# Kernel optimization log

Hardware: AMD Instinct MI355X
Metric: run time of the kernel (lower is better)

## Reference

```python
import jax, jax.numpy as jnp
import numpy as np

N, E, F_IN, EDGE_DIM = 50000, 800000, 128, 64
H, C = 4, 64  # heads, per-head out channels
NEG_SLOPE = 0.2  # PyG GATConv default


def setup_inputs() -> dict:
    key = jax.random.key(0)
    ks = jax.random.split(key, 16)
    p = lambda i, shape: jax.random.normal(ks[i], shape, jnp.float32) * 0.05
    return {
        "node_features": jax.random.normal(ks[0], (N, F_IN), jnp.float32),
        "edge_features": jax.random.normal(ks[1], (E, EDGE_DIM), jnp.float32),
        "edge_index": jax.random.randint(ks[2], (2, E), 0, N),
        # layer 1 (concat=True, ELU)
        "W1": p(3, (F_IN, H * C)),
        "att_src1": p(4, (H, C)), "att_dst1": p(5, (H, C)), "att_edge1": p(6, (H, C)),
        "bias1": jnp.zeros((H * C,), jnp.float32),
        "edgeW1": p(7, (EDGE_DIM, H * C)),
        # layer 2 (concat=False -> mean over heads, no activation)
        "W2": p(8, (H * C, H * C)),
        "att_src2": p(9, (H, C)), "att_dst2": p(10, (H, C)), "att_edge2": p(11, (H, C)),
        "bias2": jnp.zeros((C,), jnp.float32),
        "edgeW2": p(12, (EDGE_DIM, H * C)),
    }


def _gat_layer(x, edge_feat, src, dst, W, a_s, a_d, a_e, bias, edgeW, concat):
    n = x.shape[0]
    h = (x @ W).reshape(n, H, C)                      # [N,H,C]
    ef = (edge_feat @ edgeW).reshape(-1, H, C)        # [E,H,C] edge_linear projection
    # GATConv add_self_loops=True, fill_value='mean': self-loop attr = mean of incoming edge attrs
    ones = jnp.ones((src.shape[0],), x.dtype)
    cnt = jnp.maximum(jax.ops.segment_sum(ones, dst, num_segments=n), 1.0)
    loop_attr = jax.ops.segment_sum(ef, dst, num_segments=n) / cnt[:, None, None]
    ef_f = jnp.concatenate([ef, loop_attr], axis=0)   # [E+N,H,C]
    loops = jnp.arange(n)
    src_f = jnp.concatenate([src, loops], axis=0)
    dst_f = jnp.concatenate([dst, loops], axis=0)
    # per-edge attention logits: alpha_j + alpha_i + alpha_edge
    a_src = jnp.einsum('nhc,hc->nh', h, a_s)
    a_dst = jnp.einsum('nhc,hc->nh', h, a_d)
    logits = a_src[src_f] + a_dst[dst_f] + jnp.einsum('ehc,hc->eh', ef_f, a_e)
    logits = jax.nn.leaky_relu(logits, NEG_SLOPE)     # [E+N,H]
    # segment softmax over incoming edges of each dst node (every node has a self-loop)
    m = jax.ops.segment_max(logits, dst_f, num_segments=n)
    pexp = jnp.exp(logits - m[dst_f])
    denom = jax.ops.segment_sum(pexp, dst_f, num_segments=n)
    alpha = pexp / (denom[dst_f] + 1e-16)
    # message = x_j * alpha, scatter-add to dst
    out = jax.ops.segment_sum(h[src_f] * alpha[..., None], dst_f, num_segments=n)  # [N,H,C]
    if concat:
        return out.reshape(n, H * C) + bias
    return out.mean(axis=1) + bias


def reference(node_features, edge_features, edge_index,
              W1, att_src1, att_dst1, att_edge1, bias1, edgeW1,
              W2, att_src2, att_dst2, att_edge2, bias2, edgeW2):
    src, dst = edge_index[0], edge_index[1]
    x = _gat_layer(node_features, edge_features, src, dst,
                   W1, att_src1, att_dst1, att_edge1, bias1, edgeW1, concat=True)
    x = jax.nn.elu(x)
    return _gat_layer(x, edge_features, src, dst,
                      W2, att_src2, att_dst2, att_edge2, bias2, edgeW2, concat=False)
```

## Files before the change

kernel.cpp:

```cpp
#include <hip/hip_runtime.h>
#include <hip/hip_fp16.h>
#include <math.h>

#define NNODE 50000
#define NEDGE 800000
#define FIN 128
#define EDIM 64
#define HC 256
#define NH 4
#define CC 64
#define SCAN_TILE 512

typedef _Float16 half8v __attribute__((ext_vector_type(8)));
typedef _Float16 half4v __attribute__((ext_vector_type(4)));
typedef float floatx4 __attribute__((ext_vector_type(4)));

__global__ __launch_bounds__(256) void k_prep(int* counts,
                                              const float* __restrict__ W1, _Float16* wt1,
                                              const float* __restrict__ W2, _Float16* wt2,
                                              const float* __restrict__ eW1, const float* __restrict__ ae1, float* we1,
                                              const float* __restrict__ eW2, const float* __restrict__ ae2, float* we2) {
    int b = blockIdx.x, t = threadIdx.x;
    if (b < 196) {
        int i = b * 256 + t;
        if (i < NNODE) counts[i] = 0;
    } else if (b < 324) {
        int idx = (b - 196) * 256 + t;
        int n = idx >> 7, k = idx & 127;
        wt1[n * FIN + k] = (_Float16)W1[(size_t)k * HC + n];
    } else if (b < 580) {
        int idx = (b - 324) * 256 + t;
        int n = idx >> 8, k = idx & 255;
        wt2[n * HC + k] = (_Float16)W2[(size_t)k * HC + n];
    } else {
        int idx = (b - 580) * 256 + t;
        const float* eW = idx < 256 ? eW1 : eW2;
        const float* ae = idx < 256 ? ae1 : ae2;
        float* we = idx < 256 ? we1 : we2;
        int q = idx & 255;
        int d = q >> 2, hh = q & 3;
        float s = 0.f;
        for (int c = 0; c < 64; c++) s += eW[d * HC + hh * 64 + c] * ae[hh * 64 + c];
        we[d * 4 + hh] = s;
    }
}

__global__ void k_count(const int* __restrict__ dst, int* counts, int* __restrict__ rank, int E) {
    int e = blockIdx.x * 256 + threadIdx.x;
    if (e < E) rank[e] = atomicAdd(&counts[dst[e]], 1);
}

__global__ void k_scan1(const int* __restrict__ counts, int* offs, int* tilesums, int N) {
    __shared__ int s[SCAN_TILE];
    int t = threadIdx.x;
    int i = blockIdx.x * SCAN_TILE + t;
    int v = (i < N) ? counts[i] : 0;
    s[t] = v;
    for (int off = 1; off < SCAN_TILE; off <<= 1) {
        __syncthreads();
        int x = (t >= off) ? s[t - off] : 0;
        __syncthreads();
        s[t] += x;
    }
    __syncthreads();
    if (i < N) offs[i] = s[t] - v;
    if (t == SCAN_TILE - 1) tilesums[blockIdx.x] = s[t];
}

__global__ void k_scan3(int* offs, const int* __restrict__ tilesums, int nt, int N, int E) {
    __shared__ int sT[128];
    int t = threadIdx.x;
    if (t < 128) sT[t] = (t < nt) ? tilesums[t] : 0;
    __syncthreads();
    int b = blockIdx.x;
    int pre = 0;
    for (int i = 0; i < b; i++) pre += sT[i];
    int i = b * SCAN_TILE + t;
    if (i < N) offs[i] += pre;
    if (b == 0 && t == 0) offs[N] = E;
}

__device__ inline float4 h4_to_f4(uint2 r) {
    float2 fa = __half22float2(*(__half2*)&r.x);
    float2 fb = __half22float2(*(__half2*)&r.y);
    return make_float4(fa.x, fa.y, fb.x, fb.y);
}

__device__ inline float sel_h(float4 v, int head) {
    return head == 0 ? v.x : head == 1 ? v.y : head == 2 ? v.z : v.w;
}

__global__ __launch_bounds__(256) void k_edge(const int* __restrict__ src,
                                              const int* __restrict__ dst,
                                              const int* __restrict__ rank,
                                              const int* __restrict__ offs,
                                              const float* __restrict__ ef,
                                              const float* __restrict__ we1,
                                              const float* __restrict__ we2,
                                              int* __restrict__ srcs,
                                              float* __restrict__ elogc1,
                                              float* __restrict__ elogc2, int E) {
    __shared__ float sw1[256], sw2[256];
    int t = threadIdx.x;
    sw1[t] = we1[t];
    sw2[t] = we2[t];
    __syncthreads();
    int lane = t & 63, wave = t >> 6;
    int g = lane >> 2, r = lane & 3;
    int e = blockIdx.x * 64 + wave * 16 + g;
    if (e >= E) return;

    const float4* row = (const float4*)(ef + (size_t)e * EDIM);
    float4 v0 = row[r * 4 + 0];
    float4 v1 = row[r * 4 + 1];
    float4 v2 = row[r * 4 + 2];
    float4 v3 = row[r * 4 + 3];

    int pos = offs[dst[e]] + rank[e];
    int sv = src[e];

    float a10 = 0.f, a11 = 0.f, a12 = 0.f, a13 = 0.f;
    float a20 = 0.f, a21 = 0.f, a22 = 0.f, a23 = 0.f;
    int c0 = r * 16;
    const float4* vv[4] = {&v0, &v1, &v2, &v3};
#pragma unroll
    for (int q = 0; q < 4; q++) {
        const float* vp = (const float*)vv[q];
#pragma unroll
        for (int k = 0; k < 4; k++) {
            float f = vp[k];
            int c = c0 + q * 4 + k;
            float4 w1 = *(const float4*)&sw1[c << 2];
            float4 w2 = *(const float4*)&sw2[c << 2];
            a10 += f * w1.x; a11 += f * w1.y; a12 += f * w1.z; a13 += f * w1.w;
            a20 += f * w2.x; a21 += f * w2.y; a22 += f * w2.z; a23 += f * w2.w;
        }
    }
#pragma unroll
    for (int msk = 1; msk <= 2; msk <<= 1) {
        a10 += __shfl_xor(a10, msk, 64); a11 += __shfl_xor(a11, msk, 64);
        a12 += __shfl_xor(a12, msk, 64); a13 += __shfl_xor(a13, msk, 64);
        a20 += __shfl_xor(a20, msk, 64); a21 += __shfl_xor(a21, msk, 64);
        a22 += __shfl_xor(a22, msk, 64); a23 += __shfl_xor(a23, msk, 64);
    }
    if (r == 0) ((float4*)elogc1)[pos] = make_float4(a10, a11, a12, a13);
    else if (r == 1) ((float4*)elogc2)[pos] = make_float4(a20, a21, a22, a23);
    else if (r == 2) srcs[pos] = sv;
}

template <typename AT>
__global__ __launch_bounds__(256) void k_gemm_mfma(const AT* __restrict__ A,
                                                   const _Float16* __restrict__ Wt16,
                                                   _Float16* __restrict__ H16,
                                                   const float* __restrict__ att_s,
                                                   const float* __restrict__ att_d,
                                                   float* __restrict__ asrc,
                                                   float* __restrict__ adst,
                                                   int M, int K) {
    int wave = threadIdx.x >> 6, lane = threadIdx.x & 63;
    int quad = lane >> 4, l16 = lane & 15;
    int row = blockIdx.x * 64 + wave * 16 + l16;
    bool rok = row < M;
    floatx4 acc[16];
#pragma unroll
    for (int i = 0; i < 16; i++) acc[i] = (floatx4)(0.0f);
    int nk = K >> 5;
    for (int kk = 0; kk < nk; kk++) {
        half8v a = {};
        if (rok) {
            if constexpr (sizeof(AT) == 2) {
                a = *(const half8v*)(A + (size_t)row * K + kk * 32 + quad * 8);
            } else {
                const float* ap = (const float*)A + (size_t)row * K + kk * 32 + quad * 8;
                float4 v0 = *(const float4*)ap;
                float4 v1 = *(const float4*)(ap + 4);
                a[0] = (_Float16)v0.x; a[1] = (_Float16)v0.y;
                a[2] = (_Float16)v0.z; a[3] = (_Float16)v0.w;
                a[4] = (_Float16)v1.x; a[5] = (_Float16)v1.y;
                a[6] = (_Float16)v1.z; a[7] = (_Float16)v1.w;
            }
        }
#pragma unroll
        for (int nt = 0; nt < 16; nt++) {
            half8v b = *(const half8v*)(Wt16 + (size_t)(nt * 16 + l16) * K + kk * 32 + quad * 8);
            acc[nt] = __builtin_amdgcn_mfma_f32_16x16x32_f16(a, b, acc[nt], 0, 0, 0);
        }
    }
    float asl[16], adl[16];
#pragma unroll
    for (int nt = 0; nt < 16; nt++) {
        asl[nt] = att_s[nt * 16 + l16];
        adl[nt] = att_d[nt * 16 + l16];
    }
    int orow0 = blockIdx.x * 64 + wave * 16 + quad * 4;
#pragma unroll
    for (int r = 0; r < 4; r++) {
        int orow = orow0 + r;
        float4 vs4, vd4;
        float* vsp = (float*)&vs4;
        float* vdp = (float*)&vd4;
#pragma unroll
        for (int hh = 0; hh < 4; hh++) {
            float vs = 0.f, vd = 0.f;
#pragma unroll
            for (int q = 0; q < 4; q++) {
                int nt = hh * 4 + q;
                float hv = acc[nt][r];
                vs += hv * asl[nt];
                vd += hv * adl[nt];
            }
            vs += __shfl_xor(vs, 1, 64); vd += __shfl_xor(vd, 1, 64);
            vs += __shfl_xor(vs, 2, 64); vd += __shfl_xor(vd, 2, 64);
            vs += __shfl_xor(vs, 4, 64); vd += __shfl_xor(vd, 4, 64);
            vs += __shfl_xor(vs, 8, 64); vd += __shfl_xor(vd, 8, 64);
            vsp[hh] = vs; vdp[hh] = vd;
        }
        if (l16 == 0 && orow < M) {
            ((float4*)asrc)[orow] = vs4;
            ((float4*)adst)[orow] = vd4;
        }
    }
#pragma unroll
    for (int r = 0; r < 4; r++) {
        int orow = orow0 + r;
        if (orow < M) {
#pragma unroll
            for (int nt = 0; nt < 16; nt++)
                H16[(size_t)orow * HC + nt * 16 + l16] = (_Float16)acc[nt][r];
        }
    }
}

template <int LAYER>
__global__ __launch_bounds__(256) void k_aggr_fused(const _Float16* __restrict__ hb,
                                                    const float* __restrict__ elogc,
                                                    const float* __restrict__ asrc,
                                                    const float* __restrict__ adst,
                                                    const int* __restrict__ offs,
                                                    const int* __restrict__ srcs,
                                                    const float* __restrict__ bias,
                                                    _Float16* __restrict__ out16,
                                                    float* __restrict__ out32, int N) {
    __shared__ float sW[4][256];
    int wave = threadIdx.x >> 6, lane = threadIdx.x & 63;
    int n = blockIdx.x * 4 + wave;
    if (n >= N) return;
    int head = lane >> 4;
    const uint2* hf = (const uint2*)hb;
    const float4* elc = (const float4*)elogc;
    const float4* asp = (const float4*)asrc;
    float* sWp = sW[wave];
    int beg = offs[n], end = offs[n + 1];

    float4 adn = ((const float4*)adst)[n];
    float adnh = sel_h(adn, head);

    float denom = 0.f;
    float sx = 0.f, sy = 0.f, sz = 0.f, sw = 0.f;
    float ax = 0.f, ay = 0.f, az = 0.f, aw = 0.f;

    for (int i0 = beg; i0 < end; i0 += 64) {
        int m = end - i0; if (m > 64) m = 64;
        bool act = lane < m;
        int sj = 0;
        float4 el = make_float4(0.f, 0.f, 0.f, 0.f);
        float4 a4 = make_float4(0.f, 0.f, 0.f, 0.f);
        if (act) {
            uint idx = (uint)(i0 + lane);
            sj = srcs[idx];
            el = elc[idx];
            a4 = asp[(uint)sj];
        }
        sx += el.x; sy += el.y; sz += el.z; sw += el.w;
        float4 w4;
        float l;
        l = a4.x + adn.x + el.x; l = l > 0.f ? l : 0.2f * l; w4.x = act ? __expf(l) : 0.f;
        l = a4.y + adn.y + el.y; l = l > 0.f ? l : 0.2f * l; w4.y = act ? __expf(l) : 0.f;
        l = a4.z + adn.z + el.z; l = l > 0.f ? l : 0.2f * l; w4.z = act ? __expf(l) : 0.f;
        l = a4.w + adn.w + el.w; l = l > 0.f ? l : 0.2f * l; w4.w = act ? __expf(l) : 0.f;
        *(float4*)&sWp[lane << 2] = w4;
        __builtin_amdgcn_wave_barrier();

        int j = 0;
        for (; j + 16 <= m; j += 16) {
            uint2 r[16];
            float w[16];
#pragma unroll
            for (int k = 0; k < 16; k++) {
                int sk = __builtin_amdgcn_readlane(sj, j + k);
                w[k] = sWp[((j + k) << 2) + head];
                r[k] = hf[(size_t)((uint)sk * 64u) + lane];
            }
#pragma unroll
            for (int k = 0; k < 16; k++) {
                float4 h4 = h4_to_f4(r[k]);
                denom += w[k];
                ax += w[k] * h4.x; ay += w[k] * h4.y;
                az += w[k] * h4.z; aw += w[k] * h4.w;
            }
        }
        for (; j + 8 <= m; j += 8) {
            uint2 r[8];
            float w[8];
#pragma unroll
            for (int k = 0; k < 8; k++) {
                int sk = __builtin_amdgcn_readlane(sj, j + k);
                w[k] = sWp[((j + k) << 2) + head];
                r[k] = hf[(size_t)((uint)sk * 64u) + lane];
            }
#pragma unroll
            for (int k = 0; k < 8; k++) {
                float4 h4 = h4_to_f4(r[k]);
                denom += w[k];
                ax += w[k] * h4.x; ay += w[k] * h4.y;
                az += w[k] * h4.z; aw += w[k] * h4.w;
            }
        }
        for (; j < m; j++) {
            int sk = __builtin_amdgcn_readlane(sj, j);
            float wk = sWp[(j << 2) + head];
            uint2 rk = hf[(size_t)((uint)sk * 64u) + lane];
            float4 h4 = h4_to_f4(rk);
            denom += wk;
            ax += wk * h4.x; ay += wk * h4.y;
            az += wk * h4.z; aw += wk * h4.w;
        }
        __builtin_amdgcn_wave_barrier();
    }

#pragma unroll
    for (int msk = 32; msk >= 1; msk >>= 1) {
        sx += __shfl_xor(sx, msk, 64);
        sy += __shfl_xor(sy, msk, 64);
        sz += __shfl_xor(sz, msk, 64);
        sw += __shfl_xor(sw, msk, 64);
    }
    float selh = sel_h(make_float4(sx, sy, sz, sw), head);

    float cnt = (float)(end - beg);
    if (cnt < 1.f) cnt = 1.f;
    float asnh = sel_h(asp[(uint)n], head);
    float ls = asnh + adnh + selh / cnt;
    ls = ls > 0.f ? ls : 0.2f * ls;
    float ws = __expf(ls);
    denom += ws;
    float4 hn = h4_to_f4(hf[(size_t)n * 64 + lane]);
    ax += ws * hn.x; ay += ws * hn.y; az += ws * hn.z; aw += ws * hn.w;

    float inv = 1.0f / (denom + 1e-16f);
    ax *= inv; ay *= inv; az *= inv; aw *= inv;

    if (LAYER == 1) {
        float4 bv = ((const float4*)bias)[lane];
        half4v o;
        float v;
        v = ax + bv.x; o[0] = (_Float16)(v > 0.f ? v : __expf(v) - 1.0f);
        v = ay + bv.y; o[1] = (_Float16)(v > 0.f ? v : __expf(v) - 1.0f);
        v = az + bv.z; o[2] = (_Float16)(v > 0.f ? v : __expf(v) - 1.0f);
        v = aw + bv.w; o[3] = (_Float16)(v > 0.f ? v : __expf(v) - 1.0f);
        ((half4v*)(out16 + (size_t)n * HC))[lane] = o;
    } else {
        ax += __shfl_xor(ax, 16, 64); ax += __shfl_xor(ax, 32, 64);
        ay += __shfl_xor(ay, 16, 64); ay += __shfl_xor(ay, 32, 64);
        az += __shfl_xor(az, 16, 64); az += __shfl_xor(az, 32, 64);
        aw += __shfl_xor(aw, 16, 64); aw += __shfl_xor(aw, 32, 64);
        if (lane < 16) {
            float4 bv = ((const float4*)bias)[lane];
            float4 o;
            o.x = 0.25f * ax + bv.x;
            o.y = 0.25f * ay + bv.y;
            o.z = 0.25f * az + bv.z;
            o.w = 0.25f * aw + bv.w;
            ((float4*)(out32 + (size_t)n * CC))[lane] = o;
        }
    }
}

extern "C" void kernel_launch(void* const* d_in, const int* in_sizes, int n_in,
                              void* d_out, int out_size, void* d_ws, size_t ws_size,
                              hipStream_t stream) {
    const float* x   = (const float*)d_in[0];
    const float* ef  = (const float*)d_in[1];
    const int*   ei  = (const int*)d_in[2];
    const float* W1  = (const float*)d_in[3];
    const float* as1 = (const float*)d_in[4];
    const float* ad1 = (const float*)d_in[5];
    const float* ae1 = (const float*)d_in[6];
    const float* b1  = (const float*)d_in[7];
    const float* eW1 = (const float*)d_in[8];
    const float* W2  = (const float*)d_in[9];
    const float* as2 = (const float*)d_in[10];
    const float* ad2 = (const float*)d_in[11];
    const float* ae2 = (const float*)d_in[12];
    const float* b2  = (const float*)d_in[13];
    const float* eW2 = (const float*)d_in[14];
    float* out = (float*)d_out;
    const int* srcp = ei;
    const int* dstp = ei + NEDGE;

    char* w = (char*)d_ws;
    auto alloc = [&](size_t bytes) -> char* {
        char* r = w;
        w += (bytes + 255) / 256 * 256;
        return r;
    };
    _Float16* hb16  = (_Float16*)alloc((size_t)NNODE * HC * 2);
    _Float16* x216  = (_Float16*)alloc((size_t)NNODE * HC * 2);
    _Float16* wt1   = (_Float16*)alloc((size_t)HC * FIN * 2);
    _Float16* wt2   = (_Float16*)alloc((size_t)HC * HC * 2);
    float* elogc1 = (float*)alloc((size_t)NEDGE * 4 * 4);
    float* elogc2 = (float*)alloc((size_t)NEDGE * 4 * 4);
    float* asrc   = (float*)alloc((size_t)NNODE * 4 * 4);
    float* adst   = (float*)alloc((size_t)NNODE * 4 * 4);
    float* webuf1 = (float*)alloc(64 * 4 * 4);
    float* webuf2 = (float*)alloc(64 * 4 * 4);
    int* counts  = (int*)alloc((size_t)NNODE * 4);
    int* offs    = (int*)alloc((size_t)(NNODE + 1) * 4);
    int* tiles   = (int*)alloc(1024 * 4);
    int* rank    = (int*)alloc((size_t)NEDGE * 4);
    int* srcs    = (int*)alloc((size_t)NEDGE * 4);

    k_prep<<<582, 256, 0, stream>>>(counts, W1, wt1, W2, wt2,
                                    eW1, ae1, webuf1, eW2, ae2, webuf2);

    k_count<<<(NEDGE + 255) / 256, 256, 0, stream>>>(dstp, counts, rank, NEDGE);
    int nt = (NNODE + SCAN_TILE - 1) / SCAN_TILE;
    k_scan1<<<nt, SCAN_TILE, 0, stream>>>(counts, offs, tiles, NNODE);
    k_scan3<<<nt, SCAN_TILE, 0, stream>>>(offs, tiles, nt, NNODE, NEDGE);

    k_edge<<<(NEDGE + 63) / 64, 256, 0, stream>>>(srcp, dstp, rank, offs, ef,
                                                  webuf1, webuf2, srcs, elogc1, elogc2, NEDGE);

    k_gemm_mfma<float><<<(NNODE + 63) / 64, 256, 0, stream>>>(x, wt1, hb16, as1, ad1, asrc, adst, NNODE, FIN);
    k_aggr_fused<1><<<(NNODE + 3) / 4, 256, 0, stream>>>(hb16, elogc1, asrc, adst, offs, srcs, b1, x216, nullptr, NNODE);

    k_gemm_mfma<_Float16><<<(NNODE + 63) / 64, 256, 0, stream>>>(x216, wt2, hb16, as2, ad2, asrc, adst, NNODE, HC);
    k_aggr_fused<2><<<(NNODE + 3) / 4, 256, 0, stream>>>(hb16, elogc2, asrc, adst, offs, srcs, b2, nullptr, out, NNODE);
}
```

Measured before the change: 667.2 us.

## Process two destination nodes per wave with 16-byte feature gathers

The aggregation kernel now assigns one destination node to each half-wave of 32 lanes instead of one per full wave. Each lane gathers 8 fp16 features with a single 16-byte load and keeps 8 accumulators. Source indices move from readlane broadcasts to LDS, since the two halves need different indices. This is meant to give wider memory transactions and more nodes in flight, at the cost of more registers per lane and possible divergence when the two nodes have different in-degrees.

```diff
diff --git a/kernel.cpp b/kernel.cpp
--- a/kernel.cpp
+++ b/kernel.cpp
@@ -80,12 +80,6 @@
     if (b == 0 && t == 0) offs[N] = E;
 }
 
-__device__ inline float4 h4_to_f4(uint2 r) {
-    float2 fa = __half22float2(*(__half2*)&r.x);
-    float2 fb = __half22float2(*(__half2*)&r.y);
-    return make_float4(fa.x, fa.y, fb.x, fb.y);
-}
-
 __device__ inline float sel_h(float4 v, int head) {
     return head == 0 ? v.x : head == 1 ? v.y : head == 2 ? v.z : v.w;
 }
@@ -241,101 +235,122 @@
                                                     const float* __restrict__ bias,
                                                     _Float16* __restrict__ out16,
                                                     float* __restrict__ out32, int N) {
-    __shared__ float sW[4][256];
+    __shared__ float sW[4][2][32][4];
+    __shared__ int sS[4][2][32];
     int wave = threadIdx.x >> 6, lane = threadIdx.x & 63;
-    int n = blockIdx.x * 4 + wave;
+    int half = lane >> 5, hl = lane & 31;
+    int n = blockIdx.x * 8 + wave * 2 + half;
     if (n >= N) return;
-    int head = lane >> 4;
-    const uint2* hf = (const uint2*)hb;
+    int head = hl >> 3;
+    const uint4* hf4 = (const uint4*)hb;
     const float4* elc = (const float4*)elogc;
     const float4* asp = (const float4*)asrc;
-    float* sWp = sW[wave];
+    float* sWp = (float*)sW[wave][half];
+    int* sSp = sS[wave][half];
     int beg = offs[n], end = offs[n + 1];
 
     float4 adn = ((const float4*)adst)[n];
     float adnh = sel_h(adn, head);
 
     float denom = 0.f;
-    float sx = 0.f, sy = 0.f, sz = 0.f, sw = 0.f;
-    float ax = 0.f, ay = 0.f, az = 0.f, aw = 0.f;
-
-    for (int i0 = beg; i0 < end; i0 += 64) {
-        int m = end - i0; if (m > 64) m = 64;
-        bool act = lane < m;
+    float sx = 0.f, sy = 0.f, sz = 0.f, sw_ = 0.f;
+    float acc[8] = {};
+
+    for (int i0 = beg; i0 < end; i0 += 32) {
+        int m = end - i0; if (m > 32) m = 32;
+        bool act = hl < m;
         int sj = 0;
         float4 el = make_float4(0.f, 0.f, 0.f, 0.f);
         float4 a4 = make_float4(0.f, 0.f, 0.f, 0.f);
         if (act) {
-            uint idx = (uint)(i0 + lane);
+            uint idx = (uint)(i0 + hl);
             sj = srcs[idx];
             el = elc[idx];
             a4 = asp[(uint)sj];
         }
-        sx += el.x; sy += el.y; sz += el.z; sw += el.w;
+        sx += el.x; sy += el.y; sz += el.z; sw_ += el.w;
         float4 w4;
         float l;
         l = a4.x + adn.x + el.x; l = l > 0.f ? l : 0.2f * l; w4.x = act ? __expf(l) : 0.f;
         l = a4.y + adn.y + el.y; l = l > 0.f ? l : 0.2f * l; w4.y = act ? __expf(l) : 0.f;
         l = a4.z + adn.z + el.z; l = l > 0.f ? l : 0.2f * l; w4.z = act ? __expf(l) : 0.f;
         l = a4.w + adn.w + el.w; l = l > 0.f ? l : 0.2f * l; w4.w = act ? __expf(l) : 0.f;
-        *(float4*)&sWp[lane << 2] = w4;
+        *(float4*)&sWp[hl << 2] = w4;
+        sSp[hl] = sj;
         __builtin_amdgcn_wave_barrier();
 
         int j = 0;
         for (; j + 16 <= m; j += 16) {
-            uint2 r[16];
+            uint4 r[16];
             float w[16];
 #pragma unroll
             for (int k = 0; k < 16; k++) {
-                int sk = __builtin_amdgcn_readlane(sj, j + k);
+                uint sk = (uint)sSp[j + k];
                 w[k] = sWp[((j + k) << 2) + head];
-                r[k] = hf[(size_t)((uint)sk * 64u) + lane];
+                r[k] = hf4[(size_t)(sk * 32u + (uint)hl)];
             }
 #pragma unroll
             for (int k = 0; k < 16; k++) {
-                float4 h4 = h4_to_f4(r[k]);
-                denom += w[k];
-                ax += w[k] * h4.x; ay += w[k] * h4.y;
-                az += w[k] * h4.z; aw += w[k] * h4.w;
+                float w0 = w[k];
+                denom += w0;
+                float2 f0 = __half22float2(((const __half2*)&r[k])[0]);
+                float2 f1 = __half22float2(((const __half2*)&r[k])[1]);
+                float2 f2 = __half22float2(((const __half2*)&r[k])[2]);
+                float2 f3 = __half22float2(((const __half2*)&r[k])[3]);
+                acc[0] += w0 * f0.x; acc[1] += w0 * f0.y;
+                acc[2] += w0 * f1.x; acc[3] += w0 * f1.y;
+                acc[4] += w0 * f2.x; acc[5] += w0 * f2.y;
+                acc[6] += w0 * f3.x; acc[7] += w0 * f3.y;
             }
         }
         for (; j + 8 <= m; j += 8) {
-            uint2 r[8];
+            uint4 r[8];
             float w[8];
 #pragma unroll
             for (int k = 0; k < 8; k++) {
-                int sk = __builtin_amdgcn_readlane(sj, j + k);
+                uint sk = (uint)sSp[j + k];
                 w[k] = sWp[((j + k) << 2) + head];
-                r[k] = hf[(size_t)((uint)sk * 64u) + lane];
+                r[k] = hf4[(size_t)(sk * 32u + (uint)hl)];
             }
 #pragma unroll
             for (int k = 0; k < 8; k++) {
-                float4 h4 = h4_to_f4(r[k]);
-                denom += w[k];
-                ax += w[k] * h4.x; ay += w[k] * h4.y;
-                az += w[k] * h4.z; aw += w[k] * h4.w;
+                float w0 = w[k];
+                denom += w0;
+                float2 f0 = __half22float2(((const __half2*)&r[k])[0]);
+                float2 f1 = __half22float2(((const __half2*)&r[k])[1]);
+                float2 f2 = __half22float2(((const __half2*)&r[k])[2]);
+                float2 f3 = __half22float2(((const __half2*)&r[k])[3]);
+                acc[0] += w0 * f0.x; acc[1] += w0 * f0.y;
+                acc[2] += w0 * f1.x; acc[3] += w0 * f1.y;
+                acc[4] += w0 * f2.x; acc[5] += w0 * f2.y;
+                acc[6] += w0 * f3.x; acc[7] += w0 * f3.y;
             }
         }
         for (; j < m; j++) {
-            int sk = __builtin_amdgcn_readlane(sj, j);
-            float wk = sWp[(j << 2) + head];
-            uint2 rk = hf[(size_t)((uint)sk * 64u) + lane];
-            float4 h4 = h4_to_f4(rk);
-            denom += wk;
-            ax += wk * h4.x; ay += wk * h4.y;
-            az += wk * h4.z; aw += wk * h4.w;
+            uint sk = (uint)sSp[j];
+            float w0 = sWp[(j << 2) + head];
+            uint4 rk = hf4[(size_t)(sk * 32u + (uint)hl)];
+            denom += w0;
+            float2 f0 = __half22float2(((const __half2*)&rk)[0]);
+            float2 f1 = __half22float2(((const __half2*)&rk)[1]);
+            float2 f2 = __half22float2(((const __half2*)&rk)[2]);
+            float2 f3 = __half22float2(((const __half2*)&rk)[3]);
+            acc[0] += w0 * f0.x; acc[1] += w0 * f0.y;
+            acc[2] += w0 * f1.x; acc[3] += w0 * f1.y;
+            acc[4] += w0 * f2.x; acc[5] += w0 * f2.y;
+            acc[6] += w0 * f3.x; acc[7] += w0 * f3.y;
         }
         __builtin_amdgcn_wave_barrier();
     }
 
 #pragma unroll
-    for (int msk = 32; msk >= 1; msk >>= 1) {
-        sx += __shfl_xor(sx, msk, 64);
-        sy += __shfl_xor(sy, msk, 64);
-        sz += __shfl_xor(sz, msk, 64);
-        sw += __shfl_xor(sw, msk, 64);
-    }
-    float selh = sel_h(make_float4(sx, sy, sz, sw), head);
+    for (int msk = 16; msk >= 1; msk >>= 1) {
+        sx += __shfl_xor(sx, msk, 32);
+        sy += __shfl_xor(sy, msk, 32);
+        sz += __shfl_xor(sz, msk, 32);
+        sw_ += __shfl_xor(sw_, msk, 32);
+    }
+    float selh = sel_h(make_float4(sx, sy, sz, sw_), head);
 
     float cnt = (float)(end - beg);
     if (cnt < 1.f) cnt = 1.f;
@@ -344,34 +359,55 @@
     ls = ls > 0.f ? ls : 0.2f * ls;
     float ws = __expf(ls);
     denom += ws;
-    float4 hn = h4_to_f4(hf[(size_t)n * 64 + lane]);
-    ax += ws * hn.x; ay += ws * hn.y; az += ws * hn.z; aw += ws * hn.w;
+    uint4 hn = hf4[(size_t)((uint)n * 32u + (uint)hl)];
+    {
+        float2 f0 = __half22float2(((const __half2*)&hn)[0]);
+        float2 f1 = __half22float2(((const __half2*)&hn)[1]);
+        float2 f2 = __half22float2(((const __half2*)&hn)[2]);
+        float2 f3 = __half22float2(((const __half2*)&hn)[3]);
+        acc[0] += ws * f0.x; acc[1] += ws * f0.y;
+        acc[2] += ws * f1.x; acc[3] += ws * f1.y;
+        acc[4] += ws * f2.x; acc[5] += ws * f2.y;
+        acc[6] += ws * f3.x; acc[7] += ws * f3.y;
+    }
 
     float inv = 1.0f / (denom + 1e-16f);
-    ax *= inv; ay *= inv; az *= inv; aw *= inv;
+#pragma unroll
+    for (int c = 0; c < 8; c++) acc[c] *= inv;
 
     if (LAYER == 1) {
-        float4 bv = ((const float4*)bias)[lane];
-        half4v o;
-        float v;
-        v = ax + bv.x; o[0] = (_Float16)(v > 0.f ? v : __expf(v) - 1.0f);
-        v = ay + bv.y; o[1] = (_Float16)(v > 0.f ? v : __expf(v) - 1.0f);
-        v = az + bv.z; o[2] = (_Float16)(v > 0.f ? v : __expf(v) - 1.0f);
-        v = aw + bv.w; o[3] = (_Float16)(v > 0.f ? v : __expf(v) - 1.0f);
-        ((half4v*)(out16 + (size_t)n * HC))[lane] = o;
+        const float4* bp = (const float4*)bias;
+        float4 b0 = bp[hl * 2], b1 = bp[hl * 2 + 1];
+        const float* b0p = (const float*)&b0;
+        const float* b1p = (const float*)&b1;
+        half8v o;
+#pragma unroll
+        for (int c = 0; c < 4; c++) {
+            float v = acc[c] + b0p[c];
+            o[c] = (_Float16)(v > 0.f ? v : __expf(v) - 1.0f);
+        }
+#pragma unroll
+        for (int c = 0; c < 4; c++) {
+            float v = acc[4 + c] + b1p[c];
+            o[4 + c] = (_Float16)(v > 0.f ? v : __expf(v) - 1.0f);
+        }
+        ((half8v*)(out16 + (size_t)n * HC))[hl] = o;
     } else {
-        ax += __shfl_xor(ax, 16, 64); ax += __shfl_xor(ax, 32, 64);
-        ay += __shfl_xor(ay, 16, 64); ay += __shfl_xor(ay, 32, 64);
-        az += __shfl_xor(az, 16, 64); az += __shfl_xor(az, 32, 64);
-        aw += __shfl_xor(aw, 16, 64); aw += __shfl_xor(aw, 32, 64);
-        if (lane < 16) {
-            float4 bv = ((const float4*)bias)[lane];
-            float4 o;
-            o.x = 0.25f * ax + bv.x;
-            o.y = 0.25f * ay + bv.y;
-            o.z = 0.25f * az + bv.z;
-            o.w = 0.25f * aw + bv.w;
-            ((float4*)(out32 + (size_t)n * CC))[lane] = o;
+#pragma unroll
+        for (int c = 0; c < 8; c++) {
+            acc[c] += __shfl_xor(acc[c], 8, 32);
+            acc[c] += __shfl_xor(acc[c], 16, 32);
+        }
+        if (hl < 8) {
+            const float4* bp = (const float4*)bias;
+            float4 b0 = bp[hl * 2], b1 = bp[hl * 2 + 1];
+            float4 o0, o1;
+            o0.x = 0.25f * acc[0] + b0.x; o0.y = 0.25f * acc[1] + b0.y;
+            o0.z = 0.25f * acc[2] + b0.z; o0.w = 0.25f * acc[3] + b0.w;
+            o1.x = 0.25f * acc[4] + b1.x; o1.y = 0.25f * acc[5] + b1.y;
+            o1.z = 0.25f * acc[6] + b1.z; o1.w = 0.25f * acc[7] + b1.w;
+            float4* op = (float4*)(out32 + (size_t)n * CC + hl * 8);
+            op[0] = o0; op[1] = o1;
         }
     }
 }
@@ -432,8 +468,8 @@
                                                   webuf1, webuf2, srcs, elogc1, elogc2, NEDGE);
 
     k_gemm_mfma<float><<<(NNODE + 63) / 64, 256, 0, stream>>>(x, wt1, hb16, as1, ad1, asrc, adst, NNODE, FIN);
-    k_aggr_fused<1><<<(NNODE + 3) / 4, 256, 0, stream>>>(hb16, elogc1, asrc, adst, offs, srcs, b1, x216, nullptr, NNODE);
+    k_aggr_fused<1><<<(NNODE + 7) / 8, 256, 0, stream>>>(hb16, elogc1, asrc, adst, offs, srcs, b1, x216, nullptr, NNODE);
 
     k_gemm_mfma<_Float16><<<(NNODE + 63) / 64, 256, 0, stream>>>(x216, wt2, hb16, as2, ad2, asrc, adst, NNODE, HC);
-    k_aggr_fused<2><<<(NNODE + 3) / 4, 256, 0, stream>>>(hb16, elogc2, asrc, adst, offs, srcs, b2, nullptr, out, NNODE);
-}
+    k_aggr_fused<2><<<(NNODE + 7) / 8, 256, 0, stream>>>(hb16, elogc2, asrc, adst, offs, srcs, b2, nullptr, out, NNODE);
+}
```

Result: no change. 665.7 us (-0.2%).
